# Kernel tuning notes

Measured on AMD Instinct MI355X. Metric: run time of the kernel, lower is better.

## Reference

```python
import jax, jax.numpy as jnp
import numpy as np

T = 2048
D_IN = 1024
D_OUT = 1024
N_HEAD = 16
HEAD_DIM = D_OUT // N_HEAD


def setup_inputs() -> dict:
    key = jax.random.key(0)
    kx, kq, kk, kv = jax.random.split(key, 4)
    s = 1.0 / np.sqrt(D_IN)
    return {
        "x": jax.random.normal(kx, (T, D_IN), dtype=jnp.float32),
        "W_q": jax.random.normal(kq, (D_OUT, D_IN), dtype=jnp.float32) * s,
        "W_k": jax.random.normal(kk, (D_OUT, D_IN), dtype=jnp.float32) * s,
        "W_v": jax.random.normal(kv, (D_OUT, D_IN), dtype=jnp.float32) * s,
    }


def reference(x, W_q, W_k, W_v):
    t = x.shape[0]
    # linear projections (torch Linear: y = x @ W.T), split into heads: [H, T, Dh]
    q = (x @ W_q.T).reshape(t, N_HEAD, HEAD_DIM).transpose(1, 0, 2)
    k = (x @ W_k.T).reshape(t, N_HEAD, HEAD_DIM).transpose(1, 0, 2)
    v = (x @ W_v.T).reshape(t, N_HEAD, HEAD_DIM).transpose(1, 0, 2)
    # raw scores [H, T, T]
    omega = jnp.einsum("hqd,hkd->hqk", q, k)
    causal = jnp.triu(jnp.ones((t, t), dtype=bool), k=1)
    omega = jnp.where(causal[None, :, :], -jnp.inf, omega)
    # NOTE: faithful to source quirk — divides by head_dim**(-0.5),
    # i.e. multiplies scores by sqrt(head_dim)
    att_w = jax.nn.softmax(omega * (HEAD_DIM ** 0.5), axis=-1)
    context = jnp.einsum("hqk,hkd->hqd", att_w, v)  # [H, T, Dh]
    return context.transpose(1, 0, 2).reshape(t, D_OUT)
```

## Files before the change

### kernel.cpp

```cpp
#include <hip/hip_runtime.h>
#include <hip/hip_bf16.h>


typedef __bf16 bf16x8 __attribute__((ext_vector_type(8)));
typedef __bf16 bf16x4 __attribute__((ext_vector_type(4)));
typedef float  f32x4  __attribute__((ext_vector_type(4)));
typedef float  f32x16 __attribute__((ext_vector_type(16)));
typedef unsigned int u32;
typedef u32 u32x2 __attribute__((ext_vector_type(2)));
typedef u32 u32x4 __attribute__((ext_vector_type(4)));

#define MFMA(a, b, c) __builtin_amdgcn_mfma_f32_16x16x32_bf16((a), (b), (c), 0, 0, 0)
#define MFMA32(a, b, c) __builtin_amdgcn_mfma_f32_32x32x16_bf16((a), (b), (c), 0, 0, 0)

#if __has_builtin(__builtin_amdgcn_exp2f)
#define EXP2F(x) __builtin_amdgcn_exp2f(x)
#else
#define EXP2F(x) exp2f(x)
#endif

constexpr int T = 2048, DIN = 1024, DOUT = 1024, NH = 16, DH = 64;
constexpr float SC = 11.5415603f;
constexpr float DEFER = 0.6931472f;

constexpr size_t SZ_XMAT = (size_t)T * DIN * 2;
constexpr size_t SZ_WMAT = (size_t)DOUT * DIN * 2;
constexpr size_t OFF_XH = 0;
constexpr size_t OFF_XL = OFF_XH + SZ_XMAT;
constexpr size_t OFF_QH = OFF_XL + SZ_XMAT;
constexpr size_t OFF_QL = OFF_QH + SZ_XMAT;
constexpr size_t OFF_KH = OFF_QL + SZ_XMAT;
constexpr size_t OFF_KL = OFF_KH + SZ_XMAT;
constexpr size_t OFF_VT = OFF_KL + SZ_XMAT;
constexpr size_t OFF_W  = OFF_VT + SZ_XMAT;

__device__ __forceinline__ void gload_lds16(const void* g, void* l) {
  __builtin_amdgcn_global_load_lds(
      (const __attribute__((address_space(1))) void*)g,
      (__attribute__((address_space(3))) void*)l, 16, 0, 0);
}

__global__ void split_all(const float* __restrict__ x, const float* __restrict__ wq,
                          const float* __restrict__ wk, const float* __restrict__ wv,
                          char* __restrict__ ws) {
  const int i = blockIdx.x * 256 + threadIdx.x;
  const float* src;
  __bf16 *hi, *lo;
  int off;
  if (i < T * DIN / 4) {
    src = x; off = i;
    hi = (__bf16*)(ws + OFF_XH);
    lo = (__bf16*)(ws + OFF_XL);
  } else {
    const int j = i - T * DIN / 4;
    const int z = j >> 18;
    off = j & 262143;
    src = (z == 0) ? wq : ((z == 1) ? wk : wv);
    hi = (__bf16*)(ws + OFF_W + (size_t)z * 2 * SZ_WMAT);
    lo = hi + (size_t)DOUT * DIN;
  }
  const f32x4 v = ((const f32x4*)src)[off];
  bf16x4 h, l;
#pragma unroll
  for (int j = 0; j < 4; ++j) {
    const float xv = v[j];
    const __bf16 hh = (__bf16)xv;
    h[j] = hh;
    l[j] = (__bf16)(xv - (float)hh);
  }
  ((bf16x4*)hi)[off] = h;
  ((bf16x4*)lo)[off] = l;
}

template <bool SPLIT>
__device__ __forceinline__ void proj_loop(const __bf16* __restrict__ Ah,
                                          const __bf16* __restrict__ Al,
                                          const __bf16* __restrict__ Bh,
                                          const __bf16* __restrict__ Bl,
                                          __bf16* lds, int tm, int tn, int lane,
                                          int wv, f32x4 (&acc)[4][2]) {
  constexpr int BOFF = SPLIT ? 8192 : 4096;
  const int wm = wv >> 1, wn = wv & 1;
  const int q4 = lane >> 4, r16 = lane & 15;

  auto STAGE = [&](int ks) {
    const int k0 = ks * 32;
#pragma unroll
    for (int j = 0; j < 2; ++j) {
      const int cbase = wv * 64 + j * 256;
      const int c = cbase + lane;
      const int row = c & 127, kc = c >> 7;
      const size_t ga = (size_t)(tm + row) * DIN + k0 + kc * 8;
      gload_lds16(Ah + ga, lds + cbase * 8);
      if constexpr (SPLIT) gload_lds16(Al + ga, lds + 4096 + cbase * 8);
    }
    {
      const int cbase = wv * 64;
      const int c = cbase + lane;
      const int row = c & 63, kc = c >> 6;
      const size_t gb = (size_t)(tn + row) * DIN + k0 + kc * 8;
      gload_lds16(Bh + gb, lds + BOFF + cbase * 8);
      if constexpr (SPLIT) gload_lds16(Bl + gb, lds + BOFF + 2048 + cbase * 8);
    }
  };

  STAGE(0);
  for (int ks = 0; ks < 32; ++ks) {
    asm volatile("s_waitcnt vmcnt(0)" ::: "memory");
    __builtin_amdgcn_s_barrier();
    __builtin_amdgcn_sched_barrier(0);

    bf16x8 fah[4], fal[4], fbh[2], fbl[2];
#pragma unroll
    for (int b = 0; b < 4; ++b) {
      const int ra = wm * 64 + b * 16 + r16;
      fah[b] = *(const bf16x8*)(lds + (q4 * 128 + ra) * 8);
      if constexpr (SPLIT) fal[b] = *(const bf16x8*)(lds + 4096 + (q4 * 128 + ra) * 8);
    }
#pragma unroll
    for (int b = 0; b < 2; ++b) {
      const int rb = wn * 32 + b * 16 + r16;
      fbh[b] = *(const bf16x8*)(lds + BOFF + (q4 * 64 + rb) * 8);
      if constexpr (SPLIT) fbl[b] = *(const bf16x8*)(lds + BOFF + 2048 + (q4 * 64 + rb) * 8);
    }
    __builtin_amdgcn_s_setprio(1);
#pragma unroll
    for (int bm = 0; bm < 4; ++bm)
#pragma unroll
      for (int bn = 0; bn < 2; ++bn) {
        acc[bm][bn] = MFMA(fah[bm], fbh[bn], acc[bm][bn]);
        if constexpr (SPLIT) {
          acc[bm][bn] = MFMA(fah[bm], fbl[bn], acc[bm][bn]);
          acc[bm][bn] = MFMA(fal[bm], fbh[bn], acc[bm][bn]);
        }
      }
    __builtin_amdgcn_s_setprio(0);
    asm volatile("s_waitcnt lgkmcnt(0)" ::: "memory");
    __builtin_amdgcn_sched_barrier(0);
    __builtin_amdgcn_s_barrier();
    __builtin_amdgcn_sched_barrier(0);
    if (ks < 31) STAGE(ks + 1);
  }
}

__global__ __launch_bounds__(256, 3) void qkv_proj(char* ws) {
  const int bid = blockIdx.x;
  const int z = bid >> 8;
  const int t_ = bid & 255;
  const int tm = (t_ >> 4) * 128;
  const int tn = (t_ & 15) * 64;
  const int tid = threadIdx.x;
  const int lane = tid & 63, wv = tid >> 6;
  const int wm = wv >> 1, wn = wv & 1;
  const int q4 = lane >> 4, r16 = lane & 15;

  const __bf16* Ah = (const __bf16*)(ws + OFF_XH);
  const __bf16* Al = (const __bf16*)(ws + OFF_XL);
  const __bf16* Bh = (const __bf16*)(ws + OFF_W + (size_t)z * 2 * SZ_WMAT);
  const __bf16* Bl = Bh + (size_t)DOUT * DIN;

  __shared__ alignas(16) __bf16 lds[12288];

  f32x4 acc[4][2] = {};

  if (z < 2) {
    proj_loop<true>(Ah, Al, Bh, Bl, lds, tm, tn, lane, wv, acc);
    __bf16* Oh = (__bf16*)(ws + (z == 0 ? OFF_QH : OFF_KH));
    __bf16* Ol = (__bf16*)(ws + (z == 0 ? OFF_QL : OFF_KL));
#pragma unroll
    for (int bm = 0; bm < 4; ++bm)
#pragma unroll
      for (int bn = 0; bn < 2; ++bn)
#pragma unroll
        for (int r = 0; r < 4; ++r) {
          const int t = tm + wm * 64 + bm * 16 + q4 * 4 + r;
          const int n = tn + wn * 32 + bn * 16 + r16;
          const float v = acc[bm][bn][r];
          const __bf16 hh = (__bf16)v;
          Oh[(size_t)t * DOUT + n] = hh;
          Ol[(size_t)t * DOUT + n] = (__bf16)(v - (float)hh);
        }
  } else {
    proj_loop<false>(Ah, Al, Bh, Bl, lds, tm, tn, lane, wv, acc);
    __syncthreads();
    __bf16* tb = lds;
#pragma unroll
    for (int bm = 0; bm < 4; ++bm)
#pragma unroll
      for (int bn = 0; bn < 2; ++bn)
#pragma unroll
        for (int r = 0; r < 4; ++r) {
          const int tl = wm * 64 + bm * 16 + q4 * 4 + r;
          const int nl = wn * 32 + bn * 16 + r16;
          tb[(size_t)nl * 136 + tl] = (__bf16)acc[bm][bn][r];
        }
    __syncthreads();
    __bf16* Vt = (__bf16*)(ws + OFF_VT);
#pragma unroll
    for (int it = 0; it < 4; ++it) {
      const int cid = it * 256 + tid;
      const int nl = cid >> 4, tc = cid & 15;
      const bf16x8 vd = *(const bf16x8*)(tb + (size_t)nl * 136 + tc * 8);
      *(bf16x8*)(Vt + (size_t)(tn + nl) * T + tm + tc * 8) = vd;
    }
  }
}

__global__ __launch_bounds__(256, 2) void attn_kernel(const char* __restrict__ ws,
                                                      float* __restrict__ out) {
  const int bid = blockIdx.x;
  const int h = bid & 15;
  const int qt = (bid < 256) ? (31 - (bid >> 4)) : ((bid - 256) >> 4);
  const int tid = threadIdx.x;
  const int lane = tid & 63, wid = tid >> 6;
  const int qhalf = wid & 1, kvpar = wid >> 1;
  const int r32 = lane & 31, hi = lane >> 5, hi8 = hi * 8;
  const int qg = qt * 64 + qhalf * 32 + r32;
  const int NT = qt + 1;
  const int mid = (NT + 1) >> 1;
  const int tBeg = kvpar ? mid : 0;
  const int tEnd = kvpar ? NT : mid;

  const __bf16* Qh = (const __bf16*)(ws + OFF_QH);
  const __bf16* Ql = (const __bf16*)(ws + OFF_QL);
  const __bf16* Kh = (const __bf16*)(ws + OFF_KH);
  const __bf16* Kl = (const __bf16*)(ws + OFF_KL);
  const __bf16* Vt = (const __bf16*)(ws + OFF_VT);

  __shared__ alignas(16) __bf16 sK[2][2][64 * 72];

  bf16x8 fqh[4], fql[4];
#pragma unroll
  for (int ds = 0; ds < 4; ++ds) {
    const size_t off = (size_t)qg * DOUT + h * 64 + ds * 16 + hi8;
    fqh[ds] = *(const bf16x8*)(Qh + off);
    fql[ds] = *(const bf16x8*)(Ql + off);
  }

  bf16x8 st[8];
  const int hid = qhalf * 64 + lane;
  auto ISSUE = [&](int t) {
    const int kv0 = t * 64;
#pragma unroll
    for (int j = 0; j < 4; ++j) {
      const int c = j * 128 + hid;
      const int row = c >> 3, dc = c & 7;
      const size_t ko = (size_t)(kv0 + row) * DOUT + h * 64 + dc * 8;
      st[j] = *(const bf16x8*)(Kh + ko);
      st[4 + j] = *(const bf16x8*)(Kl + ko);
    }
  };
  auto WRITE = [&]() {
#pragma unroll
    for (int j = 0; j < 4; ++j) {
      const int c = j * 128 + hid;
      const int row = c >> 3, dc = c & 7;
      *(bf16x8*)(&sK[kvpar][0][row * 72 + dc * 8]) = st[j];
      *(bf16x8*)(&sK[kvpar][1][row * 72 + dc * 8]) = st[4 + j];
    }
  };

  f32x16 acc0 = {}, acc1 = {};
  float mrun = -1e30f, lrun = 0.f;

  if (tBeg < tEnd) ISSUE(tBeg);

  for (int it = 0; it < mid; ++it) {
    const int t = tBeg + it;
    const bool act = (t < tEnd);
    __builtin_amdgcn_s_barrier();
    if (act) {
      WRITE();
      if (t + 1 < tEnd) ISSUE(t + 1);
    }
    asm volatile("s_waitcnt lgkmcnt(0)" ::: "memory");
    __builtin_amdgcn_sched_barrier(0);
    __builtin_amdgcn_s_barrier();
    if (!act) continue;

    const int kv0 = t * 64;
    const bool dodiag = (t == NT - 1);
    const bool do1 = !(dodiag && qhalf == 0);

    bf16x8 va0[4], va1[4];
#pragma unroll
    for (int ks = 0; ks < 4; ++ks) {
      const size_t vo = (size_t)(h * 64 + r32) * T + kv0 + ks * 16 + hi8;
      va0[ks] = *(const bf16x8*)(Vt + vo);
      va1[ks] = *(const bf16x8*)(Vt + vo + (size_t)32 * T);
    }

    const __bf16* kbh = &sK[kvpar][0][0];
    const __bf16* kbl = &sK[kvpar][1][0];
    f32x16 s0 = {}, s1 = {};
    __builtin_amdgcn_s_setprio(1);
#pragma unroll
    for (int ds = 0; ds < 4; ++ds) {
      const int ko = ds * 16 + hi8;
      const bf16x8 kh0 = *(const bf16x8*)(kbh + r32 * 72 + ko);
      const bf16x8 kl0 = *(const bf16x8*)(kbl + r32 * 72 + ko);
      s0 = MFMA32(kh0, fqh[ds], s0);
      s0 = MFMA32(kl0, fqh[ds], s0);
      s0 = MFMA32(kh0, fql[ds], s0);
    }
    if (do1) {
#pragma unroll
      for (int ds = 0; ds < 4; ++ds) {
        const int ko = ds * 16 + hi8;
        const bf16x8 kh1 = *(const bf16x8*)(kbh + (32 + r32) * 72 + ko);
        const bf16x8 kl1 = *(const bf16x8*)(kbl + (32 + r32) * 72 + ko);
        s1 = MFMA32(kh1, fqh[ds], s1);
        s1 = MFMA32(kl1, fqh[ds], s1);
        s1 = MFMA32(kh1, fql[ds], s1);
      }
    }
    __builtin_amdgcn_s_setprio(0);

    if (dodiag) {
#pragma unroll
      for (int r = 0; r < 16; ++r) {
        const int kr = (r & 3) + 8 * (r >> 2) + 4 * hi;
        if (kv0 + kr > qg) s0[r] = -1e30f;
        if (kv0 + 32 + kr > qg) s1[r] = -1e30f;
      }
    }

    float mx = -1e30f;
#pragma unroll
    for (int r = 0; r < 16; ++r) {
      mx = fmaxf(mx, s0[r]);
      mx = fmaxf(mx, s1[r]);
    }
    mx = fmaxf(mx, __shfl_xor(mx, 32, 64));

    if (__any(mx - mrun > DEFER)) {
      const float mnew = fmaxf(mrun, mx);
      const float scale = EXP2F((mrun - mnew) * SC);
      mrun = mnew;
      lrun *= scale;
#pragma unroll
      for (int r = 0; r < 16; ++r) {
        acc0[r] *= scale;
        acc1[r] *= scale;
      }
    }
    const float mn2 = mrun * SC;

    float ps = 0.f;
#pragma unroll
    for (int r = 0; r < 16; ++r) {
      s0[r] = EXP2F(__builtin_fmaf(s0[r], SC, -mn2));
      s1[r] = EXP2F(__builtin_fmaf(s1[r], SC, -mn2));
      ps += s0[r] + s1[r];
    }
    ps += __shfl_xor(ps, 32, 64);
    lrun += ps;

    bf16x8 pb[4];
#pragma unroll
    for (int ks = 0; ks < 4; ++ks) {
      const int rb = (ks & 1) * 8;
      bf16x4 lo4, hi4;
#pragma unroll
      for (int j = 0; j < 4; ++j) {
        const float pl = (ks < 2) ? s0[rb + j] : s1[rb + j];
        const float ph = (ks < 2) ? s0[rb + 4 + j] : s1[rb + 4 + j];
        lo4[j] = (__bf16)pl;
        hi4[j] = (__bf16)ph;
      }
      const u32x2 L = __builtin_bit_cast(u32x2, lo4);
      const u32x2 H = __builtin_bit_cast(u32x2, hi4);
      u32x4 f;
#pragma unroll
      for (int q = 0; q < 2; ++q) {
        const u32 send = hi ? L[q] : H[q];
        const u32 recv = (u32)__shfl_xor((int)send, 32, 64);
        f[q] = hi ? recv : L[q];
        f[2 + q] = hi ? H[q] : recv;
      }
      pb[ks] = __builtin_bit_cast(bf16x8, f);
    }

    __builtin_amdgcn_s_setprio(1);
#pragma unroll
    for (int ks = 0; ks < 4; ++ks) {
      acc0 = MFMA32(va0[ks], pb[ks], acc0);
      acc1 = MFMA32(va1[ks], pb[ks], acc1);
    }
    __builtin_amdgcn_s_setprio(0);
  }

  __builtin_amdgcn_s_barrier();
  float* mg = (float*)&sK[0][0][0];
  if (kvpar == 1) {
    float* p = mg + (qhalf * 64 + lane) * 34;
    p[0] = mrun;
    p[1] = lrun;
#pragma unroll
    for (int r = 0; r < 16; ++r) {
      p[2 + r] = acc0[r];
      p[18 + r] = acc1[r];
    }
  }
  asm volatile("s_waitcnt lgkmcnt(0)" ::: "memory");
  __builtin_amdgcn_s_barrier();
  if (kvpar == 0) {
    const float* p = mg + (qhalf * 64 + lane) * 34;
    const float m1 = p[0], l1 = p[1];
    const float M = fmaxf(mrun, m1);
    const float w0 = EXP2F((mrun - M) * SC);
    const float w1 = EXP2F((m1 - M) * SC);
    const float rl = 1.0f / (lrun * w0 + l1 * w1);
#pragma unroll
    for (int r = 0; r < 16; ++r) {
      const int d = (r & 3) + 8 * (r >> 2) + 4 * hi;
      out[(size_t)qg * DOUT + h * 64 + d] = (acc0[r] * w0 + p[2 + r] * w1) * rl;
      out[(size_t)qg * DOUT + h * 64 + 32 + d] = (acc1[r] * w0 + p[18 + r] * w1) * rl;
    }
  }
}

extern "C" void kernel_launch(void* const* d_in, const int* in_sizes, int n_in,
                              void* d_out, int out_size, void* d_ws, size_t ws_size,
                              hipStream_t stream) {
  const float* x  = (const float*)d_in[0];
  const float* Wq = (const float*)d_in[1];
  const float* Wk = (const float*)d_in[2];
  const float* Wv = (const float*)d_in[3];
  char* ws = (char*)d_ws;

  split_all<<<5120, 256, 0, stream>>>(x, Wq, Wk, Wv, ws);
  qkv_proj<<<768, 256, 0, stream>>>(ws);
  attn_kernel<<<512, 256, 0, stream>>>(ws, (float*)d_out);
}
```

Before: 115.4 us.

## Enlarge projection tiles to 128x128 with LDS double buffering; use permlane32 swap

The QKV projection GEMM tile grows from 128x64 to 128x128 per block, halving the grid and raising arithmetic intensity per LDS fragment load. Global-to-LDS staging is double buffered with partial vmcnt waits, so the next K-slice loads while MFMAs run. In attention, cross-half lane exchanges use the permlane32_swap builtin instead of ds_bpermute shuffles. The trade-off is higher register and LDS use, fewer blocks (384) for the machine's CUs, and occupancy dropping to 2 blocks per CU.

```diff
diff --git a/kernel.cpp b/kernel.cpp
--- a/kernel.cpp
+++ b/kernel.cpp
@@ -38,6 +38,16 @@
   __builtin_amdgcn_global_load_lds(
       (const __attribute__((address_space(1))) void*)g,
       (__attribute__((address_space(3))) void*)l, 16, 0, 0);
+}
+
+__device__ __forceinline__ float xor32f(float x, int hi) {
+#if __has_builtin(__builtin_amdgcn_permlane32_swap)
+  const u32 xu = __builtin_bit_cast(u32, x);
+  const u32x2 rp = __builtin_amdgcn_permlane32_swap(xu, xu, false, false);
+  return __builtin_bit_cast(float, hi ? rp[0] : rp[1]);
+#else
+  return __shfl_xor(x, 32, 64);
+#endif
 }
 
 __global__ void split_all(const float* __restrict__ x, const float* __restrict__ wq,
@@ -78,56 +88,65 @@
                                           const __bf16* __restrict__ Bh,
                                           const __bf16* __restrict__ Bl,
                                           __bf16* lds, int tm, int tn, int lane,
-                                          int wv, f32x4 (&acc)[4][2]) {
+                                          int wv, f32x4 (&acc)[4][4]) {
+  constexpr int BUF = SPLIT ? 16384 : 8192;
   constexpr int BOFF = SPLIT ? 8192 : 4096;
   const int wm = wv >> 1, wn = wv & 1;
   const int q4 = lane >> 4, r16 = lane & 15;
 
-  auto STAGE = [&](int ks) {
+  auto STAGE = [&](int ks, int buf) {
     const int k0 = ks * 32;
+    __bf16* base = lds + buf * BUF;
 #pragma unroll
     for (int j = 0; j < 2; ++j) {
-      const int cbase = wv * 64 + j * 256;
-      const int c = cbase + lane;
-      const int row = c & 127, kc = c >> 7;
+      const int cbase = wv * 128 + j * 64;
+      const int cidx = cbase + lane;
+      const int row = cidx & 127, kc = cidx >> 7;
       const size_t ga = (size_t)(tm + row) * DIN + k0 + kc * 8;
-      gload_lds16(Ah + ga, lds + cbase * 8);
-      if constexpr (SPLIT) gload_lds16(Al + ga, lds + 4096 + cbase * 8);
-    }
-    {
-      const int cbase = wv * 64;
-      const int c = cbase + lane;
-      const int row = c & 63, kc = c >> 6;
       const size_t gb = (size_t)(tn + row) * DIN + k0 + kc * 8;
-      gload_lds16(Bh + gb, lds + BOFF + cbase * 8);
-      if constexpr (SPLIT) gload_lds16(Bl + gb, lds + BOFF + 2048 + cbase * 8);
+      gload_lds16(Ah + ga, base + cbase * 8);
+      gload_lds16(Bh + gb, base + BOFF + cbase * 8);
+      if constexpr (SPLIT) {
+        gload_lds16(Al + ga, base + 4096 + cbase * 8);
+        gload_lds16(Bl + gb, base + 12288 + cbase * 8);
+      }
     }
   };
 
-  STAGE(0);
+  STAGE(0, 0);
+  STAGE(1, 1);
+
   for (int ks = 0; ks < 32; ++ks) {
-    asm volatile("s_waitcnt vmcnt(0)" ::: "memory");
+    const int buf = ks & 1;
+    if (ks < 31) {
+      if constexpr (SPLIT) asm volatile("s_waitcnt vmcnt(8)" ::: "memory");
+      else                 asm volatile("s_waitcnt vmcnt(4)" ::: "memory");
+    } else {
+      asm volatile("s_waitcnt vmcnt(0)" ::: "memory");
+    }
     __builtin_amdgcn_s_barrier();
     __builtin_amdgcn_sched_barrier(0);
 
-    bf16x8 fah[4], fal[4], fbh[2], fbl[2];
+    const __bf16* ldsA = lds + buf * BUF;
+    const __bf16* ldsB = ldsA + BOFF;
+
+    bf16x8 fah[4], fbh[4], fal[4], fbl[4];
 #pragma unroll
     for (int b = 0; b < 4; ++b) {
       const int ra = wm * 64 + b * 16 + r16;
-      fah[b] = *(const bf16x8*)(lds + (q4 * 128 + ra) * 8);
-      if constexpr (SPLIT) fal[b] = *(const bf16x8*)(lds + 4096 + (q4 * 128 + ra) * 8);
-    }
-#pragma unroll
-    for (int b = 0; b < 2; ++b) {
-      const int rb = wn * 32 + b * 16 + r16;
-      fbh[b] = *(const bf16x8*)(lds + BOFF + (q4 * 64 + rb) * 8);
-      if constexpr (SPLIT) fbl[b] = *(const bf16x8*)(lds + BOFF + 2048 + (q4 * 64 + rb) * 8);
+      const int rb = wn * 64 + b * 16 + r16;
+      fah[b] = *(const bf16x8*)(ldsA + (q4 * 128 + ra) * 8);
+      fbh[b] = *(const bf16x8*)(ldsB + (q4 * 128 + rb) * 8);
+      if constexpr (SPLIT) {
+        fal[b] = *(const bf16x8*)(ldsA + 4096 + (q4 * 128 + ra) * 8);
+        fbl[b] = *(const bf16x8*)(ldsB + 4096 + (q4 * 128 + rb) * 8);
+      }
     }
     __builtin_amdgcn_s_setprio(1);
 #pragma unroll
     for (int bm = 0; bm < 4; ++bm)
 #pragma unroll
-      for (int bn = 0; bn < 2; ++bn) {
+      for (int bn = 0; bn < 4; ++bn) {
         acc[bm][bn] = MFMA(fah[bm], fbh[bn], acc[bm][bn]);
         if constexpr (SPLIT) {
           acc[bm][bn] = MFMA(fah[bm], fbl[bn], acc[bm][bn]);
@@ -139,16 +158,16 @@
     __builtin_amdgcn_sched_barrier(0);
     __builtin_amdgcn_s_barrier();
     __builtin_amdgcn_sched_barrier(0);
-    if (ks < 31) STAGE(ks + 1);
-  }
-}
-
-__global__ __launch_bounds__(256, 3) void qkv_proj(char* ws) {
+    if (ks < 30) STAGE(ks + 2, buf);
+  }
+}
+
+__global__ __launch_bounds__(256, 2) void qkv_proj(char* ws) {
   const int bid = blockIdx.x;
-  const int z = bid >> 8;
-  const int t_ = bid & 255;
-  const int tm = (t_ >> 4) * 128;
-  const int tn = (t_ & 15) * 64;
+  const int z = bid >> 7;
+  const int t_ = bid & 127;
+  const int tm = (t_ >> 3) * 128;
+  const int tn = (t_ & 7) * 128;
   const int tid = threadIdx.x;
   const int lane = tid & 63, wv = tid >> 6;
   const int wm = wv >> 1, wn = wv & 1;
@@ -159,9 +178,9 @@
   const __bf16* Bh = (const __bf16*)(ws + OFF_W + (size_t)z * 2 * SZ_WMAT);
   const __bf16* Bl = Bh + (size_t)DOUT * DIN;
 
-  __shared__ alignas(16) __bf16 lds[12288];
-
-  f32x4 acc[4][2] = {};
+  __shared__ alignas(16) __bf16 lds[32768];
+
+  f32x4 acc[4][4] = {};
 
   if (z < 2) {
     proj_loop<true>(Ah, Al, Bh, Bl, lds, tm, tn, lane, wv, acc);
@@ -170,11 +189,11 @@
 #pragma unroll
     for (int bm = 0; bm < 4; ++bm)
 #pragma unroll
-      for (int bn = 0; bn < 2; ++bn)
+      for (int bn = 0; bn < 4; ++bn)
 #pragma unroll
         for (int r = 0; r < 4; ++r) {
           const int t = tm + wm * 64 + bm * 16 + q4 * 4 + r;
-          const int n = tn + wn * 32 + bn * 16 + r16;
+          const int n = tn + wn * 64 + bn * 16 + r16;
           const float v = acc[bm][bn][r];
           const __bf16 hh = (__bf16)v;
           Oh[(size_t)t * DOUT + n] = hh;
@@ -187,17 +206,17 @@
 #pragma unroll
     for (int bm = 0; bm < 4; ++bm)
 #pragma unroll
-      for (int bn = 0; bn < 2; ++bn)
+      for (int bn = 0; bn < 4; ++bn)
 #pragma unroll
         for (int r = 0; r < 4; ++r) {
           const int tl = wm * 64 + bm * 16 + q4 * 4 + r;
-          const int nl = wn * 32 + bn * 16 + r16;
+          const int nl = wn * 64 + bn * 16 + r16;
           tb[(size_t)nl * 136 + tl] = (__bf16)acc[bm][bn][r];
         }
     __syncthreads();
     __bf16* Vt = (__bf16*)(ws + OFF_VT);
 #pragma unroll
-    for (int it = 0; it < 4; ++it) {
+    for (int it = 0; it < 8; ++it) {
       const int cid = it * 256 + tid;
       const int nl = cid >> 4, tc = cid & 15;
       const bf16x8 vd = *(const bf16x8*)(tb + (size_t)nl * 136 + tc * 8);
@@ -331,7 +350,7 @@
       mx = fmaxf(mx, s0[r]);
       mx = fmaxf(mx, s1[r]);
     }
-    mx = fmaxf(mx, __shfl_xor(mx, 32, 64));
+    mx = fmaxf(mx, xor32f(mx, hi));
 
     if (__any(mx - mrun > DEFER)) {
       const float mnew = fmaxf(mrun, mx);
@@ -353,7 +372,7 @@
       s1[r] = EXP2F(__builtin_fmaf(s1[r], SC, -mn2));
       ps += s0[r] + s1[r];
     }
-    ps += __shfl_xor(ps, 32, 64);
+    ps += xor32f(ps, hi);
     lrun += ps;
 
     bf16x8 pb[4];
@@ -371,6 +390,14 @@
       const u32x2 L = __builtin_bit_cast(u32x2, lo4);
       const u32x2 H = __builtin_bit_cast(u32x2, hi4);
       u32x4 f;
+#if __has_builtin(__builtin_amdgcn_permlane32_swap)
+#pragma unroll
+      for (int q = 0; q < 2; ++q) {
+        const u32x2 rp = __builtin_amdgcn_permlane32_swap(L[q], H[q], false, false);
+        f[q] = rp[0];
+        f[2 + q] = rp[1];
+      }
+#else
 #pragma unroll
       for (int q = 0; q < 2; ++q) {
         const u32 send = hi ? L[q] : H[q];
@@ -378,6 +405,7 @@
         f[q] = hi ? recv : L[q];
         f[2 + q] = hi ? H[q] : recv;
       }
+#endif
       pb[ks] = __builtin_bit_cast(bf16x8, f);
     }
 
@@ -430,6 +458,6 @@
   char* ws = (char*)d_ws;
 
   split_all<<<5120, 256, 0, stream>>>(x, Wq, Wk, Wv, ws);
-  qkv_proj<<<768, 256, 0, stream>>>(ws);
+  qkv_proj<<<384, 256, 0, stream>>>(ws);
   attn_kernel<<<512, 256, 0, stream>>>(ws, (float*)d_out);
 }
```

Result: faster. 96.22 us (-16.7%).
